# Optimization experiments

Measured on AMD Instinct MI355X. Metric: run time of the kernel, lower is better.

## Reference

```python
import jax, jax.numpy as jnp
import numpy as np

NUM_HEADS = 32
HEAD_DIM = 128
NUM_KV_HEADS = 8
Q_LEN = 1024
MAX_SEQ = 4096
CACHE_BATCH = 4
SEQ_POS = 1024
BATCH_POS = 1


def setup_inputs() -> dict:
    key = jax.random.key(0)
    ks = jax.random.split(key, 6)
    query_state = jax.random.normal(ks[0], (1, NUM_HEADS, Q_LEN, HEAD_DIM), jnp.float32)
    key_state = jax.random.normal(ks[1], (1, NUM_KV_HEADS, Q_LEN, HEAD_DIM), jnp.float32)
    value_state = jax.random.normal(ks[2], (1, NUM_KV_HEADS, Q_LEN, HEAD_DIM), jnp.float32)
    past_key_state = jax.random.normal(ks[3], (CACHE_BATCH, NUM_KV_HEADS, MAX_SEQ, HEAD_DIM), jnp.float32)
    past_value_state = jax.random.normal(ks[4], (CACHE_BATCH, NUM_KV_HEADS, MAX_SEQ, HEAD_DIM), jnp.float32)
    # Causal prefill mask: query token i (global pos SEQ_POS+i) may attend to cache pos m <= SEQ_POS+i
    i = jnp.arange(Q_LEN)[:, None] + SEQ_POS
    j = jnp.arange(MAX_SEQ)[None, :]
    attn_mask = (j <= i).astype(jnp.float32)[None, None]  # [1,1,Q_LEN,MAX_SEQ]
    scale = jnp.array([1.0 / np.sqrt(HEAD_DIM)], jnp.float32)
    return {
        "query_state": query_state,
        "key_state": key_state,
        "value_state": value_state,
        "attn_mask": attn_mask,
        "batch_position": BATCH_POS,
        "past_key_state": past_key_state,
        "past_value_state": past_value_state,
        "seq_position": SEQ_POS,
        "scale": scale,
    }


def reference(query_state, key_state, value_state, attn_mask, batch_position,
              past_key_state, past_value_state, seq_position, scale):
    g = NUM_HEADS // NUM_KV_HEADS
    q_len = query_state.shape[2]
    # --- cache update (prefill: insert new K/V at [batch_position, :, seq_position:seq_position+q_len]) ---
    k_cache = jax.lax.dynamic_update_slice(past_key_state, key_state, (batch_position, 0, seq_position, 0))
    v_cache = jax.lax.dynamic_update_slice(past_value_state, value_state, (batch_position, 0, seq_position, 0))
    # --- grouped-query attention over the updated cache row ---
    q = query_state.reshape(1, NUM_KV_HEADS, g, q_len, HEAD_DIM)
    k = jax.lax.dynamic_slice_in_dim(k_cache, batch_position, 1, axis=0)[0]  # [kvh, MAX_SEQ, hd]
    v = jax.lax.dynamic_slice_in_dim(v_cache, batch_position, 1, axis=0)[0]
    scores = jnp.einsum('bkgqd,kmd->bkgqm', q, k) * scale[0]  # [1,kvh,g,q,MAX_SEQ]
    neg = jnp.finfo(scores.dtype).min
    scores = jnp.where(attn_mask[:, :, None] > 0.5, scores, neg)
    probs = jax.nn.softmax(scores, axis=-1)
    out = jnp.einsum('bkgqm,kmd->bkgqd', probs, v)  # [1,kvh,g,q,hd]
    out = out.reshape(1, NUM_HEADS, q_len, HEAD_DIM)
    attn_output = out.transpose(0, 2, 1, 3).reshape(1, q_len, NUM_HEADS * HEAD_DIM)
    return attn_output, k_cache, v_cache
```

## Files before the change

### kernel.cpp

```cpp
#include <hip/hip_runtime.h>

#define NH 32
#define KVHN 8
#define HD 128
#define QL 1024
#define MS 4096
#define KVB 64

typedef __bf16 bf16x8 __attribute__((ext_vector_type(8)));
typedef __bf16 bf16x4 __attribute__((ext_vector_type(4)));
typedef float f32x4 __attribute__((ext_vector_type(4)));
typedef float f32x16 __attribute__((ext_vector_type(16)));


__device__ __forceinline__ void gload16(const void* g, void* l) {
    __builtin_amdgcn_global_load_lds(
        (const __attribute__((address_space(1))) unsigned int*)g,
        (__attribute__((address_space(3))) unsigned int*)l, 16, 0, 0);
}

__device__ __forceinline__ unsigned int pk2(float a, float b) {
    union { __bf16 h; unsigned short u; } x, y;
    x.h = (__bf16)a; y.h = (__bf16)b;
    return (unsigned int)x.u | ((unsigned int)y.u << 16);
}

__device__ __forceinline__ float exp2fast(float x) {
    return __builtin_amdgcn_exp2f(x);
}

__global__ __launch_bounds__(256) void cache_update_kernel(
    const float4* __restrict__ kn, const float4* __restrict__ vn,
    const float4* __restrict__ pk, const float4* __restrict__ pv,
    const int* __restrict__ bp_p, const int* __restrict__ sp_p,
    float4* __restrict__ ok, float4* __restrict__ ov,
    __bf16* __restrict__ kbf)
{
    int i = blockIdx.x * 256 + threadIdx.x;
    int bp = *bp_p, sp = *sp_p;
    int d4  = i & 31;
    int pos = (i >> 5) & 4095;
    int kvh = (i >> 17) & 7;
    int b   = i >> 20;
    float4 kv4, vv4;
    if (b == bp && pos >= sp && pos < sp + QL) {
        int ns = (kvh * QL + (pos - sp)) * 32 + d4;
        kv4 = kn[ns]; vv4 = vn[ns];
    } else {
        kv4 = pk[i]; vv4 = pv[i];
    }
    ok[i] = kv4; ov[i] = vv4;
    if (b == bp) {
        bf16x4 o;
        o[0] = (__bf16)kv4.x; o[1] = (__bf16)kv4.y;
        o[2] = (__bf16)kv4.z; o[3] = (__bf16)kv4.w;
        int c16 = d4 >> 1, half = d4 & 1;
        *(bf16x4*)(kbf + ((size_t)kvh * MS + pos) * HD
                       + ((c16 ^ (pos & 7)) * 8 + half * 4)) = o;
    }
}

__global__ __launch_bounds__(256) void v_transpose_kernel(
    const float* __restrict__ vn, const float* __restrict__ pv,
    const int* __restrict__ bp_p, const int* __restrict__ sp_p,
    __bf16* __restrict__ vt)
{
    __shared__ __bf16 tile[64][132];
    int blk = blockIdx.x;
    int kvh = blk >> 6;
    int pt  = blk & 63;
    int bp = *bp_p, sp = *sp_p;
    int r0 = threadIdx.x >> 2;
    int cb = (threadIdx.x & 3) * 32;
    int pos = pt * 64 + r0;
    const float* src = (pos >= sp && pos < sp + QL)
        ? vn + ((size_t)kvh * QL + (pos - sp)) * HD + cb
        : pv + (((size_t)(bp * KVHN) + kvh) * MS + pos) * HD + cb;
    #pragma unroll
    for (int j = 0; j < 8; ++j) {
        float4 f = *(const float4*)(src + j * 4);
        bf16x4 o;
        o[0] = (__bf16)f.x; o[1] = (__bf16)f.y; o[2] = (__bf16)f.z; o[3] = (__bf16)f.w;
        *(bf16x4*)(&tile[r0][cb + j * 4]) = o;
    }
    __syncthreads();
    #pragma unroll
    for (int p = 0; p < 4; ++p) {
        int u = threadIdx.x + p * 256;
        int d = u >> 3; int chk = u & 7;
        bf16x8 v;
        #pragma unroll
        for (int j = 0; j < 8; ++j) v[j] = tile[chk * 8 + j][d];
        *(bf16x8*)(vt + (((size_t)kvh * 64 + pt) * HD + d) * 64
                      + ((chk ^ (d & 7)) * 8)) = v;
    }
}

__global__ __launch_bounds__(256, 2) void attn_kernel(
    const float* __restrict__ q,
    const int* __restrict__ sp_p,
    const float* __restrict__ scale_p,
    const __bf16* __restrict__ kbf, const __bf16* __restrict__ vt,
    float* __restrict__ out)
{
    __shared__ __align__(16) unsigned char smem[65536];

    const int sp = *sp_p;
    const float scl = *scale_p * 1.44269504088896340736f;

    int bid = blockIdx.x;
    int kvh = bid & 7;
    int inner = (bid & 255) >> 3;
    int headLocal = inner & 3;
    int j = inner >> 2;
    int qtile = (bid < 256) ? j : 15 - j;
    int head = kvh * 4 + headLocal;

    const int q0     = qtile * 64;
    const int tid    = threadIdx.x;
    const int wave   = tid >> 6;
    const int qsub   = wave & 1;
    const int kvhalf = wave >> 1;
    const int lane   = tid & 63;
    const int hi     = lane >> 5;
    const int c31    = lane & 31;
    const int qb     = q0 + qsub * 32;
    const int myq    = qb + c31;

    const unsigned char* krow = (const unsigned char*)(kbf + (size_t)kvh * MS * HD);
    const unsigned char* vrow = (const unsigned char*)(vt + (size_t)kvh * 64 * HD * 64);

    bf16x8 qf[8];
    #pragma unroll
    for (int dc = 0; dc < 8; ++dc) {
        const float* src = q + ((size_t)(head * QL + qb + c31) * HD + dc * 16 + hi * 8);
        float4 f0 = *(const float4*)src;
        float4 f1 = *(const float4*)(src + 4);
        bf16x8 v;
        v[0]=(__bf16)(f0.x*scl); v[1]=(__bf16)(f0.y*scl);
        v[2]=(__bf16)(f0.z*scl); v[3]=(__bf16)(f0.w*scl);
        v[4]=(__bf16)(f1.x*scl); v[5]=(__bf16)(f1.y*scl);
        v[6]=(__bf16)(f1.z*scl); v[7]=(__bf16)(f1.w*scl);
        qf[dc] = v;
    }

    f32x16 acc[4];
    #pragma unroll
    for (int dsub = 0; dsub < 4; ++dsub)
        #pragma unroll
        for (int r = 0; r < 16; ++r) acc[dsub][r] = 0.f;
    float m_run = -1e30f, l_run = 0.f;

    const int n_super = (sp + q0 + 64) >> 6;

    auto stage = [&](int buf, int t) {
        const unsigned char* kt = krow + (size_t)t * 16384;
        const unsigned char* vtile = vrow + (size_t)t * 16384;
        unsigned char* kl = smem + buf * 32768;
        unsigned char* vl = kl + 16384;
        #pragma unroll
        for (int p = 0; p < 4; ++p) {
            int off = p * 4096 + tid * 16;
            gload16(kt + off, kl + off);
            gload16(vtile + off, vl + off);
        }
    };

    int cur = 0;
    stage(0, 0);
    __syncthreads();

    for (int it = 0; it < n_super; ++it) {
        const int n0 = it * KVB + kvhalf * 32;
        if (it + 1 < n_super) stage(cur ^ 1, it + 1);

        const unsigned char* Ksm = smem + cur * 32768;
        const unsigned char* Vsm = Ksm + 16384;

        f32x16 st;
        #pragma unroll
        for (int r = 0; r < 16; ++r) st[r] = 0.f;
        int kr = kvhalf * 32 + c31;
        __builtin_amdgcn_s_setprio(1);
        #pragma unroll
        for (int dc = 0; dc < 8; ++dc) {
            bf16x8 kf = *(const bf16x8*)(Ksm + kr * 256 + (((2 * dc + hi) ^ (kr & 7)) << 4));
            st = __builtin_amdgcn_mfma_f32_32x32x16_bf16(kf, qf[dc], st, 0, 0, 0);
        }
        __builtin_amdgcn_s_setprio(0);

        const bool need_mask = (n0 + 31) > (sp + qb);
        float mx = -1e30f;
        #pragma unroll
        for (int r = 0; r < 16; ++r) {
            if (need_mask) {
                int kvg = n0 + (r & 3) + 8 * (r >> 2) + 4 * hi;
                if (kvg > sp + myq) st[r] = -1e30f;
            }
            mx = fmaxf(mx, st[r]);
        }
        mx = fmaxf(mx, __shfl_xor(mx, 32));

        if (!__all(mx <= m_run + 8.0f)) {
            float nm = fmaxf(m_run, mx);
            float corr = exp2fast(m_run - nm);
            m_run = nm;
            l_run *= corr;
            #pragma unroll
            for (int r = 0; r < 16; ++r) {
                int qsrc = (r & 3) + 8 * (r >> 2) + 4 * hi;
                float cq = __shfl(corr, qsrc);
                acc[0][r] *= cq; acc[1][r] *= cq; acc[2][r] *= cq; acc[3][r] *= cq;
            }
        }

        float lsum = 0.f;
        #pragma unroll
        for (int r = 0; r < 16; ++r) {
            float pv = exp2fast(st[r] - m_run);
            st[r] = pv;
            lsum += pv;
        }
        l_run += lsum;

        unsigned int loW[4], hiW[4];
        #pragma unroll
        for (int qd = 0; qd < 2; ++qd) {
            int b = qd * 8;
            loW[qd*2+0] = pk2(st[b+0], st[b+1]);
            loW[qd*2+1] = pk2(st[b+2], st[b+3]);
            hiW[qd*2+0] = pk2(st[b+4], st[b+5]);
            hiW[qd*2+1] = pk2(st[b+6], st[b+7]);
        }
        bf16x8 pfrag[2];
        #pragma unroll
        for (int qd = 0; qd < 2; ++qd) {
            unsigned int own0 = hi ? hiW[qd*2+0] : loW[qd*2+0];
            unsigned int own1 = hi ? hiW[qd*2+1] : loW[qd*2+1];
            unsigned int xm0  = hi ? loW[qd*2+0] : hiW[qd*2+0];
            unsigned int xm1  = hi ? loW[qd*2+1] : hiW[qd*2+1];
            unsigned int rc0 = __shfl_xor(xm0, 32);
            unsigned int rc1 = __shfl_xor(xm1, 32);
            union { unsigned int u[4]; bf16x8 v; } fu;
            fu.u[0] = hi ? rc0 : own0;
            fu.u[1] = hi ? rc1 : own1;
            fu.u[2] = hi ? own0 : rc0;
            fu.u[3] = hi ? own1 : rc1;
            pfrag[qd] = fu.v;
        }

        __builtin_amdgcn_s_setprio(1);
        #pragma unroll
        for (int dsub = 0; dsub < 4; ++dsub) {
            int vr = dsub * 32 + c31;
            #pragma unroll
            for (int qd = 0; qd < 2; ++qd) {
                int ksg = kvhalf * 2 + qd;
                bf16x8 vf = *(const bf16x8*)(Vsm + vr * 128 + (((ksg * 2 + hi) ^ (vr & 7)) << 4));
                acc[dsub] = __builtin_amdgcn_mfma_f32_32x32x16_bf16(pfrag[qd], vf, acc[dsub], 0, 0, 0);
            }
        }
        __builtin_amdgcn_s_setprio(0);

        __syncthreads();
        cur ^= 1;
    }

    float l_full = l_run + __shfl_xor(l_run, 32);
    float* mlm = (float*)smem;
    float* mll = (float*)smem + 128;
    if (hi == 0) { mlm[wave * 32 + c31] = m_run; mll[wave * 32 + c31] = l_full; }
    __syncthreads();
    int pw = wave ^ 2;
    float m_o = mlm[pw * 32 + c31];
    float l_o = mll[pw * 32 + c31];
    float m_n = fmaxf(m_run, m_o);
    float sc   = exp2fast(m_run - m_n);
    float sc_o = exp2fast(m_o - m_n);
    float linv = 1.0f / (l_full * sc + l_o * sc_o);
    float* Oex = (float*)(smem + 1024) + (size_t)qsub * 32 * 128;
    if (kvhalf) {
        #pragma unroll
        for (int r = 0; r < 16; ++r) {
            int qsrc = (r & 3) + 8 * (r >> 2) + 4 * hi;
            float s = __shfl(sc, qsrc);
            #pragma unroll
            for (int dsub = 0; dsub < 4; ++dsub)
                Oex[qsrc * 128 + dsub * 32 + c31] = acc[dsub][r] * s;
        }
    }
    __syncthreads();
    if (!kvhalf) {
        #pragma unroll
        for (int r = 0; r < 16; ++r) {
            int qsrc = (r & 3) + 8 * (r >> 2) + 4 * hi;
            float s  = __shfl(sc, qsrc);
            float lq = __shfl(linv, qsrc);
            float* orow = out + (size_t)(qb + qsrc) * (NH * HD) + head * HD;
            #pragma unroll
            for (int dsub = 0; dsub < 4; ++dsub)
                orow[dsub * 32 + c31] =
                    (acc[dsub][r] * s + Oex[qsrc * 128 + dsub * 32 + c31]) * lq;
        }
    }
}

extern "C" void kernel_launch(void* const* d_in, const int* in_sizes, int n_in,
                              void* d_out, int out_size, void* d_ws, size_t ws_size,
                              hipStream_t stream)
{
    const float* q_st   = (const float*)d_in[0];
    const float* k_new  = (const float*)d_in[1];
    const float* v_new  = (const float*)d_in[2];
    const int*   bp_p   = (const int*)d_in[4];
    const float* past_k = (const float*)d_in[5];
    const float* past_v = (const float*)d_in[6];
    const int*   sp_p   = (const int*)d_in[7];
    const float* scl_p  = (const float*)d_in[8];

    float* out_attn = (float*)d_out;
    float* out_k    = out_attn + (size_t)QL * NH * HD;
    float* out_v    = out_k + (size_t)4 * KVHN * MS * HD;

    __bf16* kbf = (__bf16*)d_ws;
    __bf16* vtw = kbf + (size_t)KVHN * MS * HD;

    cache_update_kernel<<<16384, 256, 0, stream>>>(
        (const float4*)k_new, (const float4*)v_new,
        (const float4*)past_k, (const float4*)past_v,
        bp_p, sp_p, (float4*)out_k, (float4*)out_v, kbf);

    v_transpose_kernel<<<512, 256, 0, stream>>>(
        v_new, past_v, bp_p, sp_p, vtw);

    attn_kernel<<<512, 256, 0, stream>>>(
        q_st, sp_p, scl_p, kbf, vtw, out_attn);
}
```

Baseline: 109.9 us.

## Fuse V transpose into cache update, split QK accumulators, use permlane32 swap

Folds the V transpose/bf16 conversion into the cache-update kernel through a small shared tile, dropping one kernel launch and a second read of the V row. In the attention loop, QK^T is split across two independent MFMA accumulators to shorten the dependency chain. The max and sum reductions become trees, and the cross-half P exchange uses v_permlane32_swap instead of shuffles with selects. The fused kernel adds a __syncthreads to every cache-update block, and the permlane swap must produce the same fragment layout as the old shuffle code.

```diff
diff --git a/kernel.cpp b/kernel.cpp
--- a/kernel.cpp
+++ b/kernel.cpp
@@ -34,8 +34,9 @@
     const float4* __restrict__ pk, const float4* __restrict__ pv,
     const int* __restrict__ bp_p, const int* __restrict__ sp_p,
     float4* __restrict__ ok, float4* __restrict__ ov,
-    __bf16* __restrict__ kbf)
+    __bf16* __restrict__ kbf, __bf16* __restrict__ vt)
 {
+    __shared__ float vtile[8][132];
     int i = blockIdx.x * 256 + threadIdx.x;
     int bp = *bp_p, sp = *sp_p;
     int d4  = i & 31;
@@ -57,42 +58,18 @@
         int c16 = d4 >> 1, half = d4 & 1;
         *(bf16x4*)(kbf + ((size_t)kvh * MS + pos) * HD
                        + ((c16 ^ (pos & 7)) * 8 + half * 4)) = o;
-    }
-}
-
-__global__ __launch_bounds__(256) void v_transpose_kernel(
-    const float* __restrict__ vn, const float* __restrict__ pv,
-    const int* __restrict__ bp_p, const int* __restrict__ sp_p,
-    __bf16* __restrict__ vt)
-{
-    __shared__ __bf16 tile[64][132];
-    int blk = blockIdx.x;
-    int kvh = blk >> 6;
-    int pt  = blk & 63;
-    int bp = *bp_p, sp = *sp_p;
-    int r0 = threadIdx.x >> 2;
-    int cb = (threadIdx.x & 3) * 32;
-    int pos = pt * 64 + r0;
-    const float* src = (pos >= sp && pos < sp + QL)
-        ? vn + ((size_t)kvh * QL + (pos - sp)) * HD + cb
-        : pv + (((size_t)(bp * KVHN) + kvh) * MS + pos) * HD + cb;
-    #pragma unroll
-    for (int j = 0; j < 8; ++j) {
-        float4 f = *(const float4*)(src + j * 4);
-        bf16x4 o;
-        o[0] = (__bf16)f.x; o[1] = (__bf16)f.y; o[2] = (__bf16)f.z; o[3] = (__bf16)f.w;
-        *(bf16x4*)(&tile[r0][cb + j * 4]) = o;
+        *(float4*)&vtile[threadIdx.x >> 5][d4 * 4] = vv4;
     }
     __syncthreads();
-    #pragma unroll
-    for (int p = 0; p < 4; ++p) {
-        int u = threadIdx.x + p * 256;
-        int d = u >> 3; int chk = u & 7;
-        bf16x8 v;
-        #pragma unroll
-        for (int j = 0; j < 8; ++j) v[j] = tile[chk * 8 + j][d];
+    if (b == bp && threadIdx.x < 128) {
+        int d  = threadIdx.x;
+        int p0 = (blockIdx.x * 8) & 4095;
+        int pt = p0 >> 6, chk = (p0 & 63) >> 3;
+        bf16x8 o;
+        #pragma unroll
+        for (int j = 0; j < 8; ++j) o[j] = (__bf16)vtile[j][d];
         *(bf16x8*)(vt + (((size_t)kvh * 64 + pt) * HD + d) * 64
-                      + ((chk ^ (d & 7)) * 8)) = v;
+                      + ((chk ^ (d & 7)) * 8)) = o;
     }
 }
 
@@ -177,28 +154,34 @@
         const unsigned char* Ksm = smem + cur * 32768;
         const unsigned char* Vsm = Ksm + 16384;
 
-        f32x16 st;
-        #pragma unroll
-        for (int r = 0; r < 16; ++r) st[r] = 0.f;
+        f32x16 st0, st1;
+        #pragma unroll
+        for (int r = 0; r < 16; ++r) { st0[r] = 0.f; st1[r] = 0.f; }
         int kr = kvhalf * 32 + c31;
         __builtin_amdgcn_s_setprio(1);
         #pragma unroll
-        for (int dc = 0; dc < 8; ++dc) {
-            bf16x8 kf = *(const bf16x8*)(Ksm + kr * 256 + (((2 * dc + hi) ^ (kr & 7)) << 4));
-            st = __builtin_amdgcn_mfma_f32_32x32x16_bf16(kf, qf[dc], st, 0, 0, 0);
+        for (int dc = 0; dc < 4; ++dc) {
+            bf16x8 ka = *(const bf16x8*)(Ksm + kr * 256 + (((2 * dc + hi) ^ (kr & 7)) << 4));
+            st0 = __builtin_amdgcn_mfma_f32_32x32x16_bf16(ka, qf[dc], st0, 0, 0, 0);
+            bf16x8 kb = *(const bf16x8*)(Ksm + kr * 256 + (((2 * (dc + 4) + hi) ^ (kr & 7)) << 4));
+            st1 = __builtin_amdgcn_mfma_f32_32x32x16_bf16(kb, qf[dc + 4], st1, 0, 0, 0);
         }
         __builtin_amdgcn_s_setprio(0);
+        f32x16 st = st0 + st1;
 
         const bool need_mask = (n0 + 31) > (sp + qb);
-        float mx = -1e30f;
-        #pragma unroll
-        for (int r = 0; r < 16; ++r) {
-            if (need_mask) {
+        if (need_mask) {
+            #pragma unroll
+            for (int r = 0; r < 16; ++r) {
                 int kvg = n0 + (r & 3) + 8 * (r >> 2) + 4 * hi;
                 if (kvg > sp + myq) st[r] = -1e30f;
             }
-            mx = fmaxf(mx, st[r]);
-        }
+        }
+        float m01 = fmaxf(fmaxf(st[0], st[1]), fmaxf(st[2], st[3]));
+        float m23 = fmaxf(fmaxf(st[4], st[5]), fmaxf(st[6], st[7]));
+        float m45 = fmaxf(fmaxf(st[8], st[9]), fmaxf(st[10], st[11]));
+        float m67 = fmaxf(fmaxf(st[12], st[13]), fmaxf(st[14], st[15]));
+        float mx = fmaxf(fmaxf(m01, m23), fmaxf(m45, m67));
         mx = fmaxf(mx, __shfl_xor(mx, 32));
 
         if (!__all(mx <= m_run + 8.0f)) {
@@ -214,14 +197,15 @@
             }
         }
 
-        float lsum = 0.f;
-        #pragma unroll
-        for (int r = 0; r < 16; ++r) {
-            float pv = exp2fast(st[r] - m_run);
-            st[r] = pv;
-            lsum += pv;
-        }
-        l_run += lsum;
+        #pragma unroll
+        for (int r = 0; r < 16; ++r) st[r] = exp2fast(st[r] - m_run);
+        {
+            float s0 = (st[0] + st[1]) + (st[2] + st[3]);
+            float s1 = (st[4] + st[5]) + (st[6] + st[7]);
+            float s2 = (st[8] + st[9]) + (st[10] + st[11]);
+            float s3 = (st[12] + st[13]) + (st[14] + st[15]);
+            l_run += (s0 + s1) + (s2 + s3);
+        }
 
         unsigned int loW[4], hiW[4];
         #pragma unroll
@@ -235,17 +219,12 @@
         bf16x8 pfrag[2];
         #pragma unroll
         for (int qd = 0; qd < 2; ++qd) {
-            unsigned int own0 = hi ? hiW[qd*2+0] : loW[qd*2+0];
-            unsigned int own1 = hi ? hiW[qd*2+1] : loW[qd*2+1];
-            unsigned int xm0  = hi ? loW[qd*2+0] : hiW[qd*2+0];
-            unsigned int xm1  = hi ? loW[qd*2+1] : hiW[qd*2+1];
-            unsigned int rc0 = __shfl_xor(xm0, 32);
-            unsigned int rc1 = __shfl_xor(xm1, 32);
+            unsigned int a0 = loW[qd*2+0], b0 = hiW[qd*2+0];
+            unsigned int a1 = loW[qd*2+1], b1 = hiW[qd*2+1];
+            asm("v_permlane32_swap_b32 %0, %1" : "+v"(a0), "+v"(b0));
+            asm("v_permlane32_swap_b32 %0, %1" : "+v"(a1), "+v"(b1));
             union { unsigned int u[4]; bf16x8 v; } fu;
-            fu.u[0] = hi ? rc0 : own0;
-            fu.u[1] = hi ? rc1 : own1;
-            fu.u[2] = hi ? own0 : rc0;
-            fu.u[3] = hi ? own1 : rc1;
+            fu.u[0] = a0; fu.u[1] = a1; fu.u[2] = b0; fu.u[3] = b1;
             pfrag[qd] = fu.v;
         }
 
@@ -328,10 +307,7 @@
     cache_update_kernel<<<16384, 256, 0, stream>>>(
         (const float4*)k_new, (const float4*)v_new,
         (const float4*)past_k, (const float4*)past_v,
-        bp_p, sp_p, (float4*)out_k, (float4*)out_v, kbf);
-
-    v_transpose_kernel<<<512, 256, 0, stream>>>(
-        v_new, past_v, bp_p, sp_p, vtw);
+        bp_p, sp_p, (float4*)out_k, (float4*)out_v, kbf, vtw);
 
     attn_kernel<<<512, 256, 0, stream>>>(
         q_st, sp_p, scl_p, kbf, vtw, out_attn);
```

New measurement: 106.3 us. 3.2% less time.
